# Optimization experiments

Hardware: AMD Instinct MI355X
Metric: run time of the kernel (lower is better)

## Reference

```python
import jax, jax.numpy as jnp
import numpy as np

T = 2048
HIDDEN = 4096
NQ = 32
NKV = 8
HD = 128
THETA = 10000.0


def setup_inputs() -> dict:
    key = jax.random.key(0)
    ks = jax.random.split(key, 5)
    s = 1.0 / np.sqrt(HIDDEN)
    return {
        "positions": jnp.arange(T, dtype=jnp.int32),
        "hidden_states": jax.random.normal(ks[0], (T, HIDDEN), dtype=jnp.float32),
        "wq": jax.random.normal(ks[1], (HIDDEN, NQ * HD), dtype=jnp.float32) * s,
        "wk": jax.random.normal(ks[2], (HIDDEN, NKV * HD), dtype=jnp.float32) * s,
        "wv": jax.random.normal(ks[3], (HIDDEN, NKV * HD), dtype=jnp.float32) * s,
        "wo": jax.random.normal(ks[4], (NQ * HD, HIDDEN), dtype=jnp.float32) * s,
    }


def _rope_neox(x, positions):
    # x: [T, H, HD]; neox style: split halves, rotate
    half = HD // 2
    inv_freq = 1.0 / (THETA ** (jnp.arange(0, half, dtype=jnp.float32) / half))
    ang = positions.astype(jnp.float32)[:, None] * inv_freq[None, :]  # [T, half]
    cos = jnp.cos(ang)[:, None, :]  # [T, 1, half]
    sin = jnp.sin(ang)[:, None, :]
    x1, x2 = x[..., :half], x[..., half:]
    return jnp.concatenate([x1 * cos - x2 * sin, x2 * cos + x1 * sin], axis=-1)


def reference(positions, hidden_states, wq, wk, wv, wo):
    scale = HD ** -0.5
    q = (hidden_states @ wq).reshape(T, NQ, HD)
    k = (hidden_states @ wk).reshape(T, NKV, HD)
    v = (hidden_states @ wv).reshape(T, NKV, HD)
    q = _rope_neox(q, positions)
    k = _rope_neox(k, positions)
    # GQA: repeat kv heads to match q heads
    group = NQ // NKV
    k_r = jnp.repeat(k, group, axis=1)  # [T, NQ, HD]
    v_r = jnp.repeat(v, group, axis=1)
    scores = jnp.einsum('qhd,khd->hqk', q, k_r) * scale  # [NQ, T, T]
    causal = positions[:, None] >= positions[None, :]  # [T, T]
    scores = jnp.where(causal[None, :, :], scores, -jnp.inf)
    probs = jax.nn.softmax(scores, axis=-1)
    attn = jnp.einsum('hqk,khd->qhd', probs, v_r).reshape(T, NQ * HD)
    return attn @ wo
```

## Files before the change

kernel.cpp:

```cpp
#include <hip/hip_runtime.h>

#define T_SEQ  2048
#define HID    4096
#define NQH    32
#define NKVH   8
#define HDIM   128

typedef float  f32x4  __attribute__((ext_vector_type(4)));
typedef __bf16 bf16x8 __attribute__((ext_vector_type(8)));

__device__ __forceinline__ float bf2f(unsigned short u) {
  union { unsigned int i; float f; } v; v.i = ((unsigned int)u) << 16; return v.f;
}
__device__ __forceinline__ unsigned short f2bf(float f) {
  union { float f; unsigned int i; } v; v.f = f;
  unsigned int r = v.i + 0x7fffu + ((v.i >> 16) & 1u);
  return (unsigned short)(r >> 16);
}

__device__ __forceinline__ f32x4 mfma_bf16(bf16x8 a, bf16x8 b, f32x4 c) {
  return __builtin_amdgcn_mfma_f32_16x16x32_bf16(a, b, c, 0, 0, 0);
}

#define GLOAD16(g, l)                                              \
  __builtin_amdgcn_global_load_lds(                                \
      (const __attribute__((address_space(1))) void*)(g),          \
      (__attribute__((address_space(3))) void*)(l), 16, 0, 0)

__global__ void conv_f32_bf16(const float* __restrict__ in,
                              unsigned short* __restrict__ out) {
  long long i = ((long long)blockIdx.x * 256 + threadIdx.x) * 4;
  float4 v = *(const float4*)(in + i);
  union { unsigned short u[4]; uint2 p; } o;
  o.u[0] = f2bf(v.x); o.u[1] = f2bf(v.y); o.u[2] = f2bf(v.z); o.u[3] = f2bf(v.w);
  *(uint2*)(out + i) = o.p;
}

__global__ void transpose_conv(const float* __restrict__ W,
                               unsigned short* __restrict__ Wt, int K, int N) {
  __shared__ float tile[64][65];
  int n0 = blockIdx.x * 64, k0 = blockIdx.y * 64;
  int tx = threadIdx.x & 15, ty = threadIdx.x >> 4;
#pragma unroll
  for (int i = 0; i < 4; i++) {
    int k = ty + 16 * i;
    float4 f = *(const float4*)(W + (long long)(k0 + k) * N + n0 + tx * 4);
    tile[tx * 4 + 0][k] = f.x;
    tile[tx * 4 + 1][k] = f.y;
    tile[tx * 4 + 2][k] = f.z;
    tile[tx * 4 + 3][k] = f.w;
  }
  __syncthreads();
#pragma unroll
  for (int i = 0; i < 4; i++) {
    int n = ty + 16 * i;
    union { unsigned short u[4]; uint2 p; } o;
    o.u[0] = f2bf(tile[n][tx * 4 + 0]);
    o.u[1] = f2bf(tile[n][tx * 4 + 1]);
    o.u[2] = f2bf(tile[n][tx * 4 + 2]);
    o.u[3] = f2bf(tile[n][tx * 4 + 3]);
    *(uint2*)(Wt + (long long)(n0 + n) * K + k0 + tx * 4) = o.p;
  }
}

__global__ void transpose_conv_kv(const float* __restrict__ Wk,
                                  const float* __restrict__ Wv,
                                  unsigned short* __restrict__ Wt) {
  __shared__ float tile[64][65];
  const int N = NKVH * HDIM, K = HID;
  const float* W = blockIdx.z ? Wv : Wk;
  unsigned short* dst = Wt + (size_t)blockIdx.z * N * K;
  int n0 = blockIdx.x * 64, k0 = blockIdx.y * 64;
  int tx = threadIdx.x & 15, ty = threadIdx.x >> 4;
#pragma unroll
  for (int i = 0; i < 4; i++) {
    int k = ty + 16 * i;
    float4 f = *(const float4*)(W + (long long)(k0 + k) * N + n0 + tx * 4);
    tile[tx * 4 + 0][k] = f.x;
    tile[tx * 4 + 1][k] = f.y;
    tile[tx * 4 + 2][k] = f.z;
    tile[tx * 4 + 3][k] = f.w;
  }
  __syncthreads();
#pragma unroll
  for (int i = 0; i < 4; i++) {
    int n = ty + 16 * i;
    union { unsigned short u[4]; uint2 p; } o;
    o.u[0] = f2bf(tile[n][tx * 4 + 0]);
    o.u[1] = f2bf(tile[n][tx * 4 + 1]);
    o.u[2] = f2bf(tile[n][tx * 4 + 2]);
    o.u[3] = f2bf(tile[n][tx * 4 + 3]);
    *(uint2*)(dst + (long long)(n0 + n) * K + k0 + tx * 4) = o.p;
  }
}

template <int EPI>
__global__ __launch_bounds__(256) void gemm_bt(const unsigned short* __restrict__ A,
                                               const unsigned short* __restrict__ Bt,
                                               void* __restrict__ Cv,
                                               int M, int N, int K) {
  __shared__ unsigned short As[128 * 64];
  __shared__ unsigned short Bs[128 * 64];
  const int lin = blockIdx.y * gridDim.x + blockIdx.x;
  const int cpx = (gridDim.x * gridDim.y) >> 3;
  const int swz = (lin & 7) * cpx + (lin >> 3);
  const int bx = swz % gridDim.x, by = swz / gridDim.x;

  const int t = threadIdx.x;
  const int lane = t & 63, w = t >> 6;
  const int wr = w >> 1, wc = w & 1;
  const int l15 = lane & 15, lg = lane >> 4;
  const int m0 = by * 128, n0 = bx * 128;

  f32x4 acc[4][4];
#pragma unroll
  for (int i = 0; i < 4; i++)
#pragma unroll
    for (int j = 0; j < 4; j++) acc[i][j] = (f32x4){0.f, 0.f, 0.f, 0.f};

  for (int kt = 0; kt < K; kt += 64) {
    __syncthreads();
#pragma unroll
    for (int s = 0; s < 4; s++) {
      int c = t + s * 256;
      int row = c >> 3, sub = c & 7;
      GLOAD16(A + (long long)(m0 + row) * K + kt + ((sub ^ (row & 7)) * 8),
              (char*)As + (w * 64 + s * 256) * 16);
      GLOAD16(Bt + (long long)(n0 + row) * K + kt + ((sub ^ (row & 7)) * 8),
              (char*)Bs + (w * 64 + s * 256) * 16);
    }
    __syncthreads();

#pragma unroll
    for (int kk = 0; kk < 2; kk++) {
      bf16x8 af[4], bfr[4];
#pragma unroll
      for (int mi = 0; mi < 4; mi++) {
        int row = wr * 64 + mi * 16 + l15;
        af[mi] = *(const bf16x8*)(As + row * 64 + (((kk * 4 + lg) ^ (row & 7)) * 8));
      }
#pragma unroll
      for (int ni = 0; ni < 4; ni++) {
        int row = wc * 64 + ni * 16 + l15;
        bfr[ni] = *(const bf16x8*)(Bs + row * 64 + (((kk * 4 + lg) ^ (row & 7)) * 8));
      }
#pragma unroll
      for (int mi = 0; mi < 4; mi++)
#pragma unroll
        for (int ni = 0; ni < 4; ni++)
          acc[mi][ni] = mfma_bf16(af[mi], bfr[ni], acc[mi][ni]);
    }
  }

  const int row0 = m0 + wr * 64, col0 = n0 + wc * 64;
#pragma unroll
  for (int mi = 0; mi < 4; mi++)
#pragma unroll
    for (int ni = 0; ni < 4; ni++) {
      int rbase = row0 + mi * 16 + lg * 4;
      int col = col0 + ni * 16 + l15;
#pragma unroll
      for (int r = 0; r < 4; r++) {
        float v = acc[mi][ni][r];
        if (EPI == 0)
          ((unsigned short*)Cv)[(long long)(rbase + r) * N + col] = f2bf(v);
        else
          ((float*)Cv)[(long long)(rbase + r) * N + col] = v;
      }
    }
}

__global__ __launch_bounds__(256) void gemm_kv64(const unsigned short* __restrict__ A,
                                                 const unsigned short* __restrict__ Bt,
                                                 unsigned short* __restrict__ Ckv,
                                                 unsigned short* __restrict__ Cvt) {
  __shared__ unsigned short As[64 * 32];
  __shared__ unsigned short Bs[128 * 32];
  __shared__ unsigned short Tt[128 * 64];
  const int lin = blockIdx.y * gridDim.x + blockIdx.x;
  const int swz = (lin & 7) * 64 + (lin >> 3);
  const int bx = swz & 15, by = swz >> 4;

  const int t = threadIdx.x;
  const int lane = t & 63, w = t >> 6;
  const int wr = w >> 1, wc = w & 1;
  const int l15 = lane & 15, lg = lane >> 4;
  const int m0 = by * 64, n0 = bx * 128;
  const int K = HID;

  f32x4 acc[2][4];
#pragma unroll
  for (int i = 0; i < 2; i++)
#pragma unroll
    for (int j = 0; j < 4; j++) acc[i][j] = (f32x4){0.f, 0.f, 0.f, 0.f};

  const int c0 = t, c1 = t + 256;

  for (int kt = 0; kt < K; kt += 32) {
    __syncthreads();
    GLOAD16(A + (long long)(m0 + (c0 >> 2)) * K + kt + (c0 & 3) * 8,
            (char*)As + (w * 64) * 16);
    GLOAD16(Bt + (long long)(n0 + (c0 >> 2)) * K + kt + (c0 & 3) * 8,
            (char*)Bs + (w * 64) * 16);
    GLOAD16(Bt + (long long)(n0 + (c1 >> 2)) * K + kt + (c1 & 3) * 8,
            (char*)Bs + (w * 64 + 256) * 16);
    __syncthreads();

    bf16x8 af[2], bfr[4];
#pragma unroll
    for (int mi = 0; mi < 2; mi++)
      af[mi] = *(const bf16x8*)(As + (wr * 32 + mi * 16 + l15) * 32 + lg * 8);
#pragma unroll
    for (int ni = 0; ni < 4; ni++)
      bfr[ni] = *(const bf16x8*)(Bs + (wc * 64 + ni * 16 + l15) * 32 + lg * 8);
#pragma unroll
    for (int mi = 0; mi < 2; mi++)
#pragma unroll
      for (int ni = 0; ni < 4; ni++)
        acc[mi][ni] = mfma_bf16(af[mi], bfr[ni], acc[mi][ni]);
  }

  const int row0 = m0 + wr * 32, col0 = n0 + wc * 64;
  if (n0 < 1024) {
#pragma unroll
    for (int mi = 0; mi < 2; mi++)
#pragma unroll
      for (int ni = 0; ni < 4; ni++) {
        int rbase = row0 + mi * 16 + lg * 4;
        int col = col0 + ni * 16 + l15;
#pragma unroll
        for (int r = 0; r < 4; r++)
          Ckv[(long long)(rbase + r) * 1024 + col] = f2bf(acc[mi][ni][r]);
      }
  } else {
#pragma unroll
    for (int mi = 0; mi < 2; mi++)
#pragma unroll
      for (int ni = 0; ni < 4; ni++) {
        int nloc = wc * 64 + ni * 16 + l15;
#pragma unroll
        for (int r = 0; r < 4; r++) {
          int mloc = wr * 32 + mi * 16 + lg * 4 + r;
          Tt[nloc * 64 + (mloc ^ ((nloc & 7) << 3))] = f2bf(acc[mi][ni][r]);
        }
      }
    __syncthreads();
    const int nloc = t >> 1;
#pragma unroll
    for (int cc = 0; cc < 4; cc++) {
      int ci = (t & 1) * 4 + cc;
      int sc = ci ^ (nloc & 7);
      uint4 v = *(const uint4*)(Tt + nloc * 64 + sc * 8);
      *(uint4*)(Cvt + (long long)(n0 - 1024 + nloc) * T_SEQ + m0 + ci * 8) = v;
    }
  }
}

__global__ void rope_all(unsigned short* __restrict__ qb,
                         unsigned short* __restrict__ kb,
                         const int* __restrict__ positions) {
  const int w = threadIdx.x >> 6, d = threadIdx.x & 63;
  const int gid = blockIdx.x * 4 + w;
  unsigned short* row;
  int t;
  bool isq;
  if (gid < T_SEQ * NQH) {
    int h = gid & (NQH - 1); t = gid >> 5;
    row = qb + (size_t)t * (NQH * HDIM) + (size_t)h * HDIM;
    isq = true;
  } else {
    int g = gid - T_SEQ * NQH;
    int h = g & (NKVH - 1); t = g >> 3;
    row = kb + (size_t)t * (NKVH * HDIM) + (size_t)h * HDIM;
    isq = false;
  }
  double inv = exp2(-(double)d * 0.20762050593046014);
  double ang = (double)positions[t] * inv;
  double c = cos(ang), s = sin(ang);
  if (isq) { c *= 0.12751744416986895; s *= 0.12751744416986895; }
  float x1 = bf2f(row[d]), x2 = bf2f(row[d + 64]);
  row[d]      = f2bf((float)((double)x1 * c - (double)x2 * s));
  row[d + 64] = f2bf((float)((double)x2 * c + (double)x1 * s));
}

__global__ __launch_bounds__(256) void attn_kernel(const unsigned short* __restrict__ qb,
                                                   const unsigned short* __restrict__ kb,
                                                   const unsigned short* __restrict__ vt,
                                                   unsigned short* __restrict__ ab) {
  __shared__ unsigned short Ks[64 * 128];
  __shared__ unsigned short Vs[128 * 64];
  __shared__ unsigned short Ps[4][16 * 64];

  const int lin = blockIdx.y * gridDim.x + blockIdx.x;
  const int swz = (lin & 7) * 128 + (lin >> 3);
  const int bx = swz & 31;
  const int h  = swz >> 5;
  const int kvh = h >> 2;
  const int j  = 31 - bx;
  const int q0 = j * 64;
  const int t = threadIdx.x, lane = t & 63, w = t >> 6;
  const int l15 = lane & 15, lg = lane >> 4;

  bf16x8 qf[4];
#pragma unroll
  for (int kk = 0; kk < 4; kk++)
    qf[kk] = *(const bf16x8*)(qb + (long long)(q0 + w * 16 + l15) * (NQH * HDIM) +
                              h * HDIM + kk * 32 + lg * 8);

  f32x4 accO[8];
#pragma unroll
  for (int db = 0; db < 8; db++) accO[db] = (f32x4){0.f, 0.f, 0.f, 0.f};
  float mrun[4] = {-3e38f, -3e38f, -3e38f, -3e38f};
  float lrun[4] = {0.f, 0.f, 0.f, 0.f};

  const int nt = j + 1;
  for (int kt = 0; kt < nt; kt++) {
    __syncthreads();
#pragma unroll
    for (int s = 0; s < 4; s++) {
      int c = t + s * 256;
      int row = c >> 4, chk = c & 15;
      GLOAD16(kb + (long long)(kt * 64 + row) * (NKVH * HDIM) + kvh * HDIM +
                  ((chk ^ (row & 7)) * 8),
              (char*)Ks + (w * 64 + s * 256) * 16);
    }
#pragma unroll
    for (int s = 0; s < 4; s++) {
      int c = t + s * 256;
      int row = c >> 3, chk = c & 7;
      GLOAD16(vt + (long long)(kvh * HDIM + row) * T_SEQ + kt * 64 +
                  ((chk ^ (row & 7)) * 8),
              (char*)Vs + (w * 64 + s * 256) * 16);
    }
    __syncthreads();

    f32x4 accS[4];
#pragma unroll
    for (int kc = 0; kc < 4; kc++) accS[kc] = (f32x4){0.f, 0.f, 0.f, 0.f};
    __builtin_amdgcn_s_setprio(1);
#pragma unroll
    for (int kk = 0; kk < 4; kk++)
#pragma unroll
      for (int kc = 0; kc < 4; kc++) {
        int row = kc * 16 + l15;
        bf16x8 b = *(const bf16x8*)(Ks + row * 128 + (((kk * 4 + lg) ^ (l15 & 7)) * 8));
        accS[kc] = mfma_bf16(qf[kk], b, accS[kc]);
      }
    __builtin_amdgcn_s_setprio(0);

    float pm[4][4];
    if (kt == j) {
#pragma unroll
      for (int kc = 0; kc < 4; kc++) {
        int kcl = kc * 16 + l15;
#pragma unroll
        for (int r = 0; r < 4; r++)
          pm[kc][r] = (kcl > w * 16 + lg * 4 + r) ? -3e38f : accS[kc][r];
      }
    } else {
#pragma unroll
      for (int kc = 0; kc < 4; kc++)
#pragma unroll
        for (int r = 0; r < 4; r++) pm[kc][r] = accS[kc][r];
    }

    float rm[4];
#pragma unroll
    for (int r = 0; r < 4; r++)
      rm[r] = fmaxf(fmaxf(pm[0][r], pm[1][r]), fmaxf(pm[2][r], pm[3][r]));
    int needl = 0;
#pragma unroll
    for (int r = 0; r < 4; r++) needl |= (rm[r] > mrun[r] + 8.f) ? 1 : 0;
    if (__any(needl)) {
#pragma unroll
      for (int off = 1; off < 16; off <<= 1)
#pragma unroll
        for (int r = 0; r < 4; r++) rm[r] = fmaxf(rm[r], __shfl_xor(rm[r], off, 64));
#pragma unroll
      for (int r = 0; r < 4; r++) {
        float mn = fmaxf(mrun[r], rm[r]);
        float corr = exp2f(mrun[r] - mn);
        mrun[r] = mn;
        lrun[r] *= corr;
#pragma unroll
        for (int db = 0; db < 8; db++) accO[db][r] *= corr;
      }
    }

    __bf16 pbh[4][4];
#pragma unroll
    for (int kc = 0; kc < 4; kc++)
#pragma unroll
      for (int r = 0; r < 4; r++) {
        float p = exp2f(pm[kc][r] - mrun[r]);
        lrun[r] += p;
        pbh[kc][r] = (__bf16)p;
      }

    unsigned short* Pw = &Ps[w][0];
#pragma unroll
    for (int kc = 0; kc < 4; kc++)
#pragma unroll
      for (int r = 0; r < 4; r++) {
        int prow = lg * 4 + r;
        ((__bf16*)Pw)[(prow * 64 + kc * 16 + l15) ^ ((prow & 7) << 3)] = pbh[kc][r];
      }
    asm volatile("s_waitcnt lgkmcnt(0)" ::: "memory");

    __builtin_amdgcn_s_setprio(1);
#pragma unroll
    for (int ks = 0; ks < 2; ks++) {
      bf16x8 pa = *(const bf16x8*)(Pw + ((l15 * 64 + ks * 32 + lg * 8) ^ ((l15 & 7) << 3)));
#pragma unroll
      for (int db = 0; db < 8; db++) {
        int vrow = db * 16 + l15;
        bf16x8 b = *(const bf16x8*)(Vs + vrow * 64 + (((ks * 4 + lg) ^ (l15 & 7)) * 8));
        accO[db] = mfma_bf16(pa, b, accO[db]);
      }
    }
    __builtin_amdgcn_s_setprio(0);
  }

#pragma unroll
  for (int off = 1; off < 16; off <<= 1)
#pragma unroll
    for (int r = 0; r < 4; r++) lrun[r] += __shfl_xor(lrun[r], off, 64);
#pragma unroll
  for (int db = 0; db < 8; db++)
#pragma unroll
    for (int r = 0; r < 4; r++) {
      int qr = q0 + w * 16 + lg * 4 + r;
      int col = h * HDIM + db * 16 + l15;
      ((__bf16*)ab)[(long long)qr * (NQH * HDIM) + col] = (__bf16)(accO[db][r] / lrun[r]);
    }
}

extern "C" void kernel_launch(void* const* d_in, const int* in_sizes, int n_in,
                              void* d_out, int out_size, void* d_ws, size_t ws_size,
                              hipStream_t stream) {
  const int*   positions = (const int*)d_in[0];
  const float* hs = (const float*)d_in[1];
  const float* wq = (const float*)d_in[2];
  const float* wk = (const float*)d_in[3];
  const float* wv = (const float*)d_in[4];
  const float* wo = (const float*)d_in[5];
  float* out = (float*)d_out;

  const size_t SZ_WT = (size_t)HID * HID * 2;
  const size_t SZ_HB = (size_t)T_SEQ * HID * 2;
  const size_t SZ_QB = (size_t)T_SEQ * NQH * HDIM * 2;
  const size_t SZ_KB = (size_t)T_SEQ * NKVH * HDIM * 2;
  const size_t need = SZ_WT + SZ_HB + SZ_QB + SZ_KB * 2;
  if (ws_size < need) return;

  char* p = (char*)d_ws;
  unsigned short* wt  = (unsigned short*)p; p += SZ_WT;
  unsigned short* hb  = (unsigned short*)p; p += SZ_HB;
  unsigned short* qb  = (unsigned short*)p; p += SZ_QB;
  unsigned short* kb  = (unsigned short*)p; p += SZ_KB;
  unsigned short* vtb = (unsigned short*)p; p += SZ_KB;
  unsigned short* ab  = hb;

  conv_f32_bf16<<<(T_SEQ * HID) / 1024, 256, 0, stream>>>(hs, hb);

  transpose_conv<<<dim3((NQH * HDIM) / 64, HID / 64), 256, 0, stream>>>(wq, wt, HID, NQH * HDIM);
  gemm_bt<0><<<dim3((NQH * HDIM) / 128, T_SEQ / 128), 256, 0, stream>>>(hb, wt, qb, T_SEQ, NQH * HDIM, HID);

  transpose_conv_kv<<<dim3((NKVH * HDIM) / 64, HID / 64, 2), 256, 0, stream>>>(wk, wv, wt);
  gemm_kv64<<<dim3(16, 32), 256, 0, stream>>>(hb, wt, kb, vtb);

  rope_all<<<(T_SEQ * (NQH + NKVH)) / 4, 256, 0, stream>>>(qb, kb, positions);

  attn_kernel<<<dim3(32, 32), 256, 0, stream>>>(qb, kb, vtb, ab);

  transpose_conv<<<dim3(HID / 64, (NQH * HDIM) / 64), 256, 0, stream>>>(wo, wt, NQH * HDIM, HID);
  gemm_bt<2><<<dim3(HID / 128, T_SEQ / 128), 256, 0, stream>>>(ab, wt, out, T_SEQ, HID, NQH * HDIM);
}
```

Measured before the change: 404.9 us.

## Double K-tile depth in KV GEMM with XOR-swizzled LDS; alternate attention block order

The KV projection GEMM now stages 64-wide K slices instead of 32, halving the loop iterations and barrier pairs. It applies an XOR swizzle on 16-byte chunks to avoid LDS bank conflicts on the fragment reads. The attention kernel also reverses the query-block order for odd heads, so heavy and light causal blocks are mixed across the launch order. The trade-offs are more LDS per block and changed scheduling balance.

```diff
diff --git a/kernel.cpp b/kernel.cpp
--- a/kernel.cpp
+++ b/kernel.cpp
@@ -174,8 +174,8 @@
                                                  const unsigned short* __restrict__ Bt,
                                                  unsigned short* __restrict__ Ckv,
                                                  unsigned short* __restrict__ Cvt) {
-  __shared__ unsigned short As[64 * 32];
-  __shared__ unsigned short Bs[128 * 32];
+  __shared__ unsigned short As[64 * 64];
+  __shared__ unsigned short Bs[128 * 64];
   __shared__ unsigned short Tt[128 * 64];
   const int lin = blockIdx.y * gridDim.x + blockIdx.x;
   const int swz = (lin & 7) * 64 + (lin >> 3);
@@ -194,30 +194,43 @@
 #pragma unroll
     for (int j = 0; j < 4; j++) acc[i][j] = (f32x4){0.f, 0.f, 0.f, 0.f};
 
-  const int c0 = t, c1 = t + 256;
-
-  for (int kt = 0; kt < K; kt += 32) {
-    __syncthreads();
-    GLOAD16(A + (long long)(m0 + (c0 >> 2)) * K + kt + (c0 & 3) * 8,
-            (char*)As + (w * 64) * 16);
-    GLOAD16(Bt + (long long)(n0 + (c0 >> 2)) * K + kt + (c0 & 3) * 8,
-            (char*)Bs + (w * 64) * 16);
-    GLOAD16(Bt + (long long)(n0 + (c1 >> 2)) * K + kt + (c1 & 3) * 8,
-            (char*)Bs + (w * 64 + 256) * 16);
-    __syncthreads();
-
-    bf16x8 af[2], bfr[4];
-#pragma unroll
-    for (int mi = 0; mi < 2; mi++)
-      af[mi] = *(const bf16x8*)(As + (wr * 32 + mi * 16 + l15) * 32 + lg * 8);
-#pragma unroll
-    for (int ni = 0; ni < 4; ni++)
-      bfr[ni] = *(const bf16x8*)(Bs + (wc * 64 + ni * 16 + l15) * 32 + lg * 8);
-#pragma unroll
-    for (int mi = 0; mi < 2; mi++)
-#pragma unroll
-      for (int ni = 0; ni < 4; ni++)
-        acc[mi][ni] = mfma_bf16(af[mi], bfr[ni], acc[mi][ni]);
+  for (int kt = 0; kt < K; kt += 64) {
+    __syncthreads();
+#pragma unroll
+    for (int s = 0; s < 2; s++) {
+      int c = t + s * 256;
+      int row = c >> 3, sub = c & 7;
+      GLOAD16(A + (long long)(m0 + row) * K + kt + ((sub ^ (row & 7)) * 8),
+              (char*)As + (w * 64 + s * 256) * 16);
+    }
+#pragma unroll
+    for (int s = 0; s < 4; s++) {
+      int c = t + s * 256;
+      int row = c >> 3, sub = c & 7;
+      GLOAD16(Bt + (long long)(n0 + row) * K + kt + ((sub ^ (row & 7)) * 8),
+              (char*)Bs + (w * 64 + s * 256) * 16);
+    }
+    __syncthreads();
+
+#pragma unroll
+    for (int kk = 0; kk < 2; kk++) {
+      bf16x8 af[2], bfr[4];
+#pragma unroll
+      for (int mi = 0; mi < 2; mi++) {
+        int row = wr * 32 + mi * 16 + l15;
+        af[mi] = *(const bf16x8*)(As + row * 64 + (((kk * 4 + lg) ^ (row & 7)) * 8));
+      }
+#pragma unroll
+      for (int ni = 0; ni < 4; ni++) {
+        int row = wc * 64 + ni * 16 + l15;
+        bfr[ni] = *(const bf16x8*)(Bs + row * 64 + (((kk * 4 + lg) ^ (row & 7)) * 8));
+      }
+#pragma unroll
+      for (int mi = 0; mi < 2; mi++)
+#pragma unroll
+        for (int ni = 0; ni < 4; ni++)
+          acc[mi][ni] = mfma_bf16(af[mi], bfr[ni], acc[mi][ni]);
+    }
   }
 
   const int row0 = m0 + wr * 32, col0 = n0 + wc * 64;
@@ -296,7 +309,7 @@
   const int bx = swz & 31;
   const int h  = swz >> 5;
   const int kvh = h >> 2;
-  const int j  = 31 - bx;
+  const int j  = (h & 1) ? bx : 31 - bx;
   const int q0 = j * 64;
   const int t = threadIdx.x, lane = t & 63, w = t >> 6;
   const int l15 = lane & 15, lg = lane >> 4;
```

Result: no change. 399.9 us (-1.2%).
